# Kernel tuning notes

Measured on AMD Instinct MI355X. Metric: run time of the kernel, lower is better.

The kernel has to match this reference:

```python
import jax, jax.numpy as jnp
import numpy as np

B, D, K, L, C = 1024, 512, 255, 256, 80  # batch, feat, internal nodes, leaves, classes
DEPTH = 8  # complete binary tree: 2^8 = 256 leaves


def _build_res_path():
    # res_path[l, k] = 1 if internal node k is on leaf l's path and leaf goes left,
    # -1 if it goes right, 0 if node k not on the path (matches build_tree_squeeze).
    rp = np.zeros((L, K), dtype=np.int32)
    for leaf in range(L):
        node = 0
        for d in range(DEPTH):
            bit = (leaf >> (DEPTH - 1 - d)) & 1  # 0 -> left, 1 -> right
            rp[leaf, node] = 1 if bit == 0 else -1
            node = 2 * node + 1 + bit
    return jnp.asarray(rp)


def setup_inputs() -> dict:
    key = jax.random.key(0)
    k1, k2, k3, k4 = jax.random.split(key, 4)
    x = jax.random.normal(k1, (B, D), dtype=jnp.float32)
    node_embeddings = jax.random.normal(k2, (K, D), dtype=jnp.float32)
    leaf_W = jax.random.normal(k3, (L * C, D), dtype=jnp.float32) * (1.0 / np.sqrt(D))
    leaf_b = jax.random.normal(k4, (L * C,), dtype=jnp.float32) * 0.01
    res_path = _build_res_path()
    return {"x": x, "node_embeddings": node_embeddings, "leaf_W": leaf_W,
            "leaf_b": leaf_b, "res_path": res_path}


def reference(x, node_embeddings, leaf_W, leaf_b, res_path):
    # L2-normalize node embeddings, cosine-sim routing probabilities
    ne = node_embeddings / jnp.linalg.norm(node_embeddings, axis=-1, keepdims=True)
    node_sim = jax.nn.sigmoid(jnp.einsum('bc,kc->bk', x, ne))  # [B, K]
    # leaf decision logits: Linear(D, L*C) reshaped to [B, L, C]
    leaf_dec = (jnp.einsum('bc,oc->bo', x, leaf_W) + leaf_b).reshape(x.shape[0], L, C)
    left_mask = (res_path == 1)[None]    # [1, L, K]
    right_mask = (res_path == -1)[None]  # [1, L, K]
    ns = node_sim[:, None, :]            # [B, 1, K]
    prob_left = jnp.prod(jnp.where(left_mask, ns, 1.0), axis=-1)        # [B, L]
    prob_right = jnp.prod(jnp.where(right_mask, 1.0 - ns, 1.0), axis=-1)  # [B, L]
    probs = (prob_left * prob_right)[..., None] * leaf_dec  # [B, L, C]
    return probs.sum(axis=1), node_sim
```

## Files before the change

### kernel.cpp

```cpp
#include <hip/hip_runtime.h>
#include <stdint.h>

#define B_  1024
#define D_  512
#define K_  255
#define L_  256
#define C_  80

typedef __attribute__((ext_vector_type(8))) short bf16x8;
typedef __attribute__((ext_vector_type(4))) float f32x4;
typedef __attribute__((ext_vector_type(8))) short short8;

#define GLD(gsrc, ldst) \
  __builtin_amdgcn_global_load_lds((const __attribute__((address_space(1))) void*)(gsrc), \
                                   (__attribute__((address_space(3))) void*)(ldst), 16, 0, 0)

__device__ __forceinline__ short cvt_bf16(float f) {
    unsigned u = __float_as_uint(f);
    u += 0x7FFFu + ((u >> 16) & 1u);
    return (short)(u >> 16);
}

__global__ __launch_bounds__(256) void convert_kernel(const float* __restrict__ w,
                                                      const float* __restrict__ x,
                                                      const float* __restrict__ ne,
                                                      short* __restrict__ wb,
                                                      short* __restrict__ xb,
                                                      short* __restrict__ neb) {
    __shared__ float red[256];
    const int tid = threadIdx.x;
    if (blockIdx.x < 2048) {
        size_t i0 = (size_t)blockIdx.x * 256 + tid;
        const size_t stride = 2048u * 256u;
        for (size_t v = i0; v < 1310720u; v += stride) {
            float4 a = ((const float4*)w)[v * 2];
            float4 b = ((const float4*)w)[v * 2 + 1];
            short8 o;
            o[0] = cvt_bf16(a.x); o[1] = cvt_bf16(a.y); o[2] = cvt_bf16(a.z); o[3] = cvt_bf16(a.w);
            o[4] = cvt_bf16(b.x); o[5] = cvt_bf16(b.y); o[6] = cvt_bf16(b.z); o[7] = cvt_bf16(b.w);
            ((short8*)wb)[v] = o;
        }
        for (size_t v = i0; v < 65536u; v += stride) {
            float4 a = ((const float4*)x)[v * 2];
            float4 b = ((const float4*)x)[v * 2 + 1];
            short8 o;
            o[0] = cvt_bf16(a.x); o[1] = cvt_bf16(a.y); o[2] = cvt_bf16(a.z); o[3] = cvt_bf16(a.w);
            o[4] = cvt_bf16(b.x); o[5] = cvt_bf16(b.y); o[6] = cvt_bf16(b.z); o[7] = cvt_bf16(b.w);
            ((short8*)xb)[v] = o;
        }
    } else {
        const int row = blockIdx.x - 2048;
        if (row == 255) {
            ((unsigned*)(neb + 255 * 512))[tid] = 0u;
            return;
        }
        const float2* nr = (const float2*)(ne + (size_t)row * 512);
        float2 a = nr[tid];
        red[tid] = a.x * a.x + a.y * a.y;
        __syncthreads();
        #pragma unroll
        for (int s = 128; s > 0; s >>= 1) {
            if (tid < s) red[tid] += red[tid + s];
            __syncthreads();
        }
        float inv = rsqrtf(red[0]);
        unsigned lo = (unsigned short)cvt_bf16(a.x * inv);
        unsigned hi = (unsigned short)cvt_bf16(a.y * inv);
        ((unsigned*)(neb + (size_t)row * 512))[tid] = lo | (hi << 16);
    }
}

__global__ __launch_bounds__(256) void simgemm_kernel(const short* __restrict__ xb,
                                                      const short* __restrict__ neb,
                                                      float* __restrict__ out1) {
    __shared__ __align__(16) short Ald[512 * 8];
    __shared__ __align__(16) short Bld[512 * 8];
    const int tid = threadIdx.x;
    const int lane = tid & 63, wave = tid >> 6;
    const int q = lane >> 4, r = lane & 15;
    const int mt = blockIdx.x >> 2;
    const int nt = blockIdx.x & 3;

    f32x4 acc[4];
    #pragma unroll
    for (int nf = 0; nf < 4; ++nf) acc[nf] = (f32x4){0.f, 0.f, 0.f, 0.f};

    const bf16x8* Av = (const bf16x8*)Ald;
    const bf16x8* Bv = (const bf16x8*)Bld;

    for (int kb = 0; kb < 8; ++kb) {
        __syncthreads();
        #pragma unroll
        for (int j = 0; j < 2; ++j) {
            int ph = j * 256 + tid, rr = ph >> 3, g = (ph & 7) ^ (rr & 7);
            GLD(xb + ((size_t)(mt * 64 + rr) * D_ + kb * 64 + g * 8), Ald + ph * 8);
        }
        #pragma unroll
        for (int j = 0; j < 2; ++j) {
            int ph = j * 256 + tid, cc = ph >> 3, g = (ph & 7) ^ (cc & 7);
            GLD(neb + ((size_t)(nt * 64 + cc) * D_ + kb * 64 + g * 8), Bld + ph * 8);
        }
        __syncthreads();
        #pragma unroll
        for (int ks = 0; ks < 2; ++ks) {
            const int g = ks * 4 + q;
            int rl = wave * 16 + r;
            bf16x8 af = Av[rl * 8 + (g ^ (rl & 7))];
            #pragma unroll
            for (int nf = 0; nf < 4; ++nf) {
                int cl = nf * 16 + r;
                bf16x8 bfr = Bv[cl * 8 + (g ^ (cl & 7))];
                acc[nf] = __builtin_amdgcn_mfma_f32_16x16x32_bf16(af, bfr, acc[nf], 0, 0, 0);
            }
        }
    }
    #pragma unroll
    for (int nf = 0; nf < 4; ++nf) {
        int gcol = nt * 64 + nf * 16 + r;
        if (gcol < K_) {
            #pragma unroll
            for (int i = 0; i < 4; ++i) {
                int grow = mt * 64 + wave * 16 + q * 4 + i;
                out1[(size_t)grow * K_ + gcol] = 1.f / (1.f + __expf(-acc[nf][i]));
            }
        }
    }
}

__global__ __launch_bounds__(256) void leafprob_kernel(const float* __restrict__ out1,
                                                       float* __restrict__ p_ws) {
    __shared__ float ss[K_];
    const int b = blockIdx.x, t = threadIdx.x;
    if (t < K_) ss[t] = out1[(size_t)b * K_ + t];
    __syncthreads();
    float prob = 1.f;
    int node = 0;
    #pragma unroll
    for (int d = 0; d < 8; ++d) {
        int bit = (t >> (7 - d)) & 1;
        float s = ss[node];
        prob *= bit ? (1.f - s) : s;
        node = 2 * node + 1 + bit;
    }
    p_ws[(size_t)b * L_ + t] = prob;
}

__global__ __launch_bounds__(256, 2) void gemm_kernel(const short* __restrict__ xb,
                                                      const short* __restrict__ wb,
                                                      const float* __restrict__ p,
                                                      const float* __restrict__ lb,
                                                      float* __restrict__ partial) {
    __shared__ __align__(16) short Ald[1024 * 8];
    __shared__ __align__(16) short Bld[1280 * 8];
    __shared__ float p_ld[128][2];
    __shared__ float b_ld[160];

    const int tid = threadIdx.x;
    const int lane = tid & 63, wave = tid >> 6;
    const int q = lane >> 4, r = lane & 15;
    const int wrow = wave * 32;
    const int lp = blockIdx.x & 127;
    const int mt = blockIdx.x >> 7;

    if (tid < 128) {
        p_ld[tid][0] = p[(size_t)(mt * 128 + tid) * L_ + 2 * lp];
        p_ld[tid][1] = p[(size_t)(mt * 128 + tid) * L_ + 2 * lp + 1];
    }
    if (tid < 160) b_ld[tid] = lb[lp * 160 + tid];

    f32x4 outacc[2][5];
    #pragma unroll
    for (int mf = 0; mf < 2; ++mf)
        #pragma unroll
        for (int nf = 0; nf < 5; ++nf)
            outacc[mf][nf] = (f32x4){0.f, 0.f, 0.f, 0.f};

    const bf16x8* Av = (const bf16x8*)Ald;
    const bf16x8* Bv = (const bf16x8*)Bld;

    for (int kb = 0; kb < 8; ++kb) {
        __syncthreads();
        #pragma unroll
        for (int j = 0; j < 4; ++j) {
            int ph = j * 256 + tid;
            int rr = ph >> 3;
            int g  = (ph & 7) ^ (rr & 7);
            GLD(xb + ((size_t)(mt * 128 + rr) * D_ + kb * 64 + g * 8), Ald + ph * 8);
        }
        #pragma unroll
        for (int j = 0; j < 5; ++j) {
            int ph = j * 256 + tid;
            int cc = ph >> 3;
            int g  = (ph & 7) ^ (cc & 7);
            GLD(wb + ((size_t)(lp * 160 + cc) * D_ + kb * 64 + g * 8), Bld + ph * 8);
        }
        __syncthreads();

        #pragma unroll
        for (int li = 0; li < 2; ++li) {
            f32x4 dec[2][5];
            #pragma unroll
            for (int mf = 0; mf < 2; ++mf)
                #pragma unroll
                for (int nf = 0; nf < 5; ++nf)
                    dec[mf][nf] = (f32x4){0.f, 0.f, 0.f, 0.f};

            #pragma unroll
            for (int ks = 0; ks < 2; ++ks) {
                const int g = ks * 4 + q;
                bf16x8 af[2], bfr[5];
                #pragma unroll
                for (int mf = 0; mf < 2; ++mf) {
                    int rl = wrow + mf * 16 + r;
                    af[mf] = Av[rl * 8 + (g ^ (rl & 7))];
                }
                #pragma unroll
                for (int nf = 0; nf < 5; ++nf) {
                    int cl = li * 80 + nf * 16 + r;
                    bfr[nf] = Bv[cl * 8 + (g ^ (cl & 7))];
                }
                #pragma unroll
                for (int mf = 0; mf < 2; ++mf)
                    #pragma unroll
                    for (int nf = 0; nf < 5; ++nf)
                        dec[mf][nf] = __builtin_amdgcn_mfma_f32_16x16x32_bf16(
                            af[mf], bfr[nf], dec[mf][nf], 0, 0, 0);
            }

            #pragma unroll
            for (int mf = 0; mf < 2; ++mf)
                #pragma unroll
                for (int nf = 0; nf < 5; ++nf)
                    #pragma unroll
                    for (int i = 0; i < 4; ++i) {
                        int row = wrow + mf * 16 + q * 4 + i;
                        outacc[mf][nf][i] += p_ld[row][li] * dec[mf][nf][i];
                    }
        }
    }

    const size_t rbase = (size_t)lp * B_ + mt * 128;
    #pragma unroll
    for (int mf = 0; mf < 2; ++mf)
        #pragma unroll
        for (int nf = 0; nf < 5; ++nf) {
            int col = nf * 16 + r;
            float b0 = b_ld[col], b1 = b_ld[80 + col];
            #pragma unroll
            for (int i = 0; i < 4; ++i) {
                int row = wrow + mf * 16 + q * 4 + i;
                float v = outacc[mf][nf][i] + p_ld[row][0] * b0 + p_ld[row][1] * b1;
                partial[(rbase + row) * C_ + col] = v;
            }
        }
}

__global__ __launch_bounds__(256) void reduce_kernel(const float* __restrict__ partial,
                                                     float* __restrict__ out0) {
    int idx = blockIdx.x * 256 + threadIdx.x;
    const float4* p4 = (const float4*)partial;
    float4 s = {0.f, 0.f, 0.f, 0.f};
    #pragma unroll 8
    for (int j = 0; j < 128; ++j) {
        float4 v = p4[(size_t)j * (B_ * C_ / 4) + idx];
        s.x += v.x; s.y += v.y; s.z += v.z; s.w += v.w;
    }
    ((float4*)out0)[idx] = s;
}

extern "C" void kernel_launch(void* const* d_in, const int* in_sizes, int n_in,
                              void* d_out, int out_size, void* d_ws, size_t ws_size,
                              hipStream_t stream) {
    const float* x  = (const float*)d_in[0];
    const float* ne = (const float*)d_in[1];
    const float* lW = (const float*)d_in[2];
    const float* lb = (const float*)d_in[3];

    float* out0 = (float*)d_out;
    float* out1 = out0 + (size_t)B_ * C_;

    char* ws = (char*)d_ws;
    short* xb      = (short*)ws;
    short* neb     = (short*)(ws + (1u << 20));
    float* p_ws    = (float*)(ws + (1u << 20) + (1u << 18));
    short* wb      = (short*)(ws + (9u << 18));
    float* partial = (float*)(ws + (24u << 20));

    convert_kernel<<<2304, 256, 0, stream>>>(lW, x, ne, wb, xb, neb);
    simgemm_kernel<<<64, 256, 0, stream>>>(xb, neb, out1);
    leafprob_kernel<<<B_, 256, 0, stream>>>(out1, p_ws);
    gemm_kernel<<<1024, 256, 0, stream>>>(xb, wb, p_ws, lb, partial);
    reduce_kernel<<<B_ * C_ / 1024, 256, 0, stream>>>(partial, out0);
}
```

Before: 143.5 us.

## Drop LDS staging in leaf GEMM; load MFMA fragments directly from global memory

Removes the shared-memory tiles and their barriers from the leaf GEMM. Each wave now loads its bf16 A/B fragments directly from global memory and keeps the routing probabilities in registers. The per-chunk MFMA accumulation is replaced by a zero-initialised MFMA per 32-wide k-step, with the probability scaling applied after every step. Occupancy is raised to 3 blocks per SM. The change relies on L1/L2 to serve operand reuse across waves and trades a short accumulation chain for many more scaling FMAs and uncoalesced 16-byte gathers.

```diff
diff --git a/kernel.cpp b/kernel.cpp
--- a/kernel.cpp
+++ b/kernel.cpp
@@ -145,28 +145,31 @@
     p_ws[(size_t)b * L_ + t] = prob;
 }
 
-__global__ __launch_bounds__(256, 2) void gemm_kernel(const short* __restrict__ xb,
+__global__ __launch_bounds__(256, 3) void gemm_kernel(const short* __restrict__ xb,
                                                       const short* __restrict__ wb,
                                                       const float* __restrict__ p,
                                                       const float* __restrict__ lb,
                                                       float* __restrict__ partial) {
-    __shared__ __align__(16) short Ald[1024 * 8];
-    __shared__ __align__(16) short Bld[1280 * 8];
-    __shared__ float p_ld[128][2];
-    __shared__ float b_ld[160];
-
-    const int tid = threadIdx.x;
+    const int tid  = threadIdx.x;
     const int lane = tid & 63, wave = tid >> 6;
     const int q = lane >> 4, r = lane & 15;
     const int wrow = wave * 32;
     const int lp = blockIdx.x & 127;
     const int mt = blockIdx.x >> 7;
 
-    if (tid < 128) {
-        p_ld[tid][0] = p[(size_t)(mt * 128 + tid) * L_ + 2 * lp];
-        p_ld[tid][1] = p[(size_t)(mt * 128 + tid) * L_ + 2 * lp + 1];
-    }
-    if (tid < 160) b_ld[tid] = lb[lp * 160 + tid];
+    float pv[2][2][4];
+    #pragma unroll
+    for (int mf = 0; mf < 2; ++mf)
+        #pragma unroll
+        for (int i = 0; i < 4; ++i) {
+            const float* pr = p + (size_t)(mt * 128 + wrow + mf * 16 + q * 4 + i) * L_ + 2 * lp;
+            pv[mf][0][i] = pr[0];
+            pv[mf][1][i] = pr[1];
+        }
+
+    const short* Ab = xb + (size_t)(mt * 128 + wrow) * D_;
+    const short* Bb = wb + (size_t)lp * 160 * D_;
+    const int voff = r * D_ + q * 8;
 
     f32x4 outacc[2][5];
     #pragma unroll
@@ -175,82 +178,46 @@
         for (int nf = 0; nf < 5; ++nf)
             outacc[mf][nf] = (f32x4){0.f, 0.f, 0.f, 0.f};
 
-    const bf16x8* Av = (const bf16x8*)Ald;
-    const bf16x8* Bv = (const bf16x8*)Bld;
-
-    for (int kb = 0; kb < 8; ++kb) {
-        __syncthreads();
-        #pragma unroll
-        for (int j = 0; j < 4; ++j) {
-            int ph = j * 256 + tid;
-            int rr = ph >> 3;
-            int g  = (ph & 7) ^ (rr & 7);
-            GLD(xb + ((size_t)(mt * 128 + rr) * D_ + kb * 64 + g * 8), Ald + ph * 8);
-        }
-        #pragma unroll
-        for (int j = 0; j < 5; ++j) {
-            int ph = j * 256 + tid;
-            int cc = ph >> 3;
-            int g  = (ph & 7) ^ (cc & 7);
-            GLD(wb + ((size_t)(lp * 160 + cc) * D_ + kb * 64 + g * 8), Bld + ph * 8);
-        }
-        __syncthreads();
-
+    const f32x4 z = {0.f, 0.f, 0.f, 0.f};
+
+    #pragma unroll
+    for (int ks = 0; ks < 16; ++ks) {
+        bf16x8 af[2];
+        #pragma unroll
+        for (int mf = 0; mf < 2; ++mf)
+            af[mf] = *(const bf16x8*)(Ab + mf * 16 * D_ + ks * 32 + voff);
         #pragma unroll
         for (int li = 0; li < 2; ++li) {
-            f32x4 dec[2][5];
+            bf16x8 bfr[5];
+            #pragma unroll
+            for (int nf = 0; nf < 5; ++nf)
+                bfr[nf] = *(const bf16x8*)(Bb + (li * 80 + nf * 16) * D_ + ks * 32 + voff);
             #pragma unroll
             for (int mf = 0; mf < 2; ++mf)
                 #pragma unroll
-                for (int nf = 0; nf < 5; ++nf)
-                    dec[mf][nf] = (f32x4){0.f, 0.f, 0.f, 0.f};
-
-            #pragma unroll
-            for (int ks = 0; ks < 2; ++ks) {
-                const int g = ks * 4 + q;
-                bf16x8 af[2], bfr[5];
-                #pragma unroll
-                for (int mf = 0; mf < 2; ++mf) {
-                    int rl = wrow + mf * 16 + r;
-                    af[mf] = Av[rl * 8 + (g ^ (rl & 7))];
+                for (int nf = 0; nf < 5; ++nf) {
+                    f32x4 dec = __builtin_amdgcn_mfma_f32_16x16x32_bf16(
+                        af[mf], bfr[nf], z, 0, 0, 0);
+                    #pragma unroll
+                    for (int i = 0; i < 4; ++i)
+                        outacc[mf][nf][i] += pv[mf][li][i] * dec[i];
                 }
-                #pragma unroll
-                for (int nf = 0; nf < 5; ++nf) {
-                    int cl = li * 80 + nf * 16 + r;
-                    bfr[nf] = Bv[cl * 8 + (g ^ (cl & 7))];
-                }
-                #pragma unroll
-                for (int mf = 0; mf < 2; ++mf)
-                    #pragma unroll
-                    for (int nf = 0; nf < 5; ++nf)
-                        dec[mf][nf] = __builtin_amdgcn_mfma_f32_16x16x32_bf16(
-                            af[mf], bfr[nf], dec[mf][nf], 0, 0, 0);
-            }
-
-            #pragma unroll
-            for (int mf = 0; mf < 2; ++mf)
-                #pragma unroll
-                for (int nf = 0; nf < 5; ++nf)
-                    #pragma unroll
-                    for (int i = 0; i < 4; ++i) {
-                        int row = wrow + mf * 16 + q * 4 + i;
-                        outacc[mf][nf][i] += p_ld[row][li] * dec[mf][nf][i];
-                    }
-        }
-    }
-
+        }
+    }
+
+    const float* lbb = lb + lp * 160;
     const size_t rbase = (size_t)lp * B_ + mt * 128;
     #pragma unroll
     for (int mf = 0; mf < 2; ++mf)
         #pragma unroll
         for (int nf = 0; nf < 5; ++nf) {
             int col = nf * 16 + r;
-            float b0 = b_ld[col], b1 = b_ld[80 + col];
+            float b0 = lbb[col], b1 = lbb[80 + col];
             #pragma unroll
             for (int i = 0; i < 4; ++i) {
                 int row = wrow + mf * 16 + q * 4 + i;
-                float v = outacc[mf][nf][i] + p_ld[row][0] * b0 + p_ld[row][1] * b1;
-                partial[(rbase + row) * C_ + col] = v;
+                partial[(rbase + row) * C_ + col] =
+                    outacc[mf][nf][i] + pv[mf][0][i] * b0 + pv[mf][1][i] * b1;
             }
         }
 }
```

New measurement: 200.7 us. 39.9% more time.

## Split leaves across waves, accumulate full-K per leaf, combine pair via LDS

Applied to the files above, without the earlier changes.

Each wave now owns one leaf of the pair and 64 rows. It accumulates the full-K product in registers instead of re-zeroing per k-block and scaling by the leaf probability every block. The two leaves are combined at the end through an LDS scratch buffer that aliases the staging tiles. This removes the per-k-block probability multiply-add work, but it raises accumulator registers from 10 to 20 f32x4 and adds an LDS round trip and extra syncs in the epilogue. It also changes B-fragment reuse, with A fragments now loaded for 4 row tiles per wave.

```diff
diff --git a/kernel.cpp b/kernel.cpp
--- a/kernel.cpp
+++ b/kernel.cpp
@@ -150,15 +150,18 @@
                                                       const float* __restrict__ p,
                                                       const float* __restrict__ lb,
                                                       float* __restrict__ partial) {
-    __shared__ __align__(16) short Ald[1024 * 8];
-    __shared__ __align__(16) short Bld[1280 * 8];
+    __shared__ __align__(16) union {
+        struct { short A[1024 * 8]; short Bst[1280 * 8]; } s;
+        float scr[2][64][81];
+    } u;
     __shared__ float p_ld[128][2];
     __shared__ float b_ld[160];
 
     const int tid = threadIdx.x;
     const int lane = tid & 63, wave = tid >> 6;
     const int q = lane >> 4, r = lane & 15;
-    const int wrow = wave * 32;
+    const int li = wave >> 1;
+    const int wr = (wave & 1) * 64;
     const int lp = blockIdx.x & 127;
     const int mt = blockIdx.x >> 7;
 
@@ -168,15 +171,15 @@
     }
     if (tid < 160) b_ld[tid] = lb[lp * 160 + tid];
 
-    f32x4 outacc[2][5];
-    #pragma unroll
-    for (int mf = 0; mf < 2; ++mf)
+    f32x4 dec[4][5];
+    #pragma unroll
+    for (int mf = 0; mf < 4; ++mf)
         #pragma unroll
         for (int nf = 0; nf < 5; ++nf)
-            outacc[mf][nf] = (f32x4){0.f, 0.f, 0.f, 0.f};
-
-    const bf16x8* Av = (const bf16x8*)Ald;
-    const bf16x8* Bv = (const bf16x8*)Bld;
+            dec[mf][nf] = (f32x4){0.f, 0.f, 0.f, 0.f};
+
+    const bf16x8* Av = (const bf16x8*)u.s.A;
+    const bf16x8* Bv = (const bf16x8*)u.s.Bst;
 
     for (int kb = 0; kb < 8; ++kb) {
         __syncthreads();
@@ -185,74 +188,78 @@
             int ph = j * 256 + tid;
             int rr = ph >> 3;
             int g  = (ph & 7) ^ (rr & 7);
-            GLD(xb + ((size_t)(mt * 128 + rr) * D_ + kb * 64 + g * 8), Ald + ph * 8);
+            GLD(xb + ((size_t)(mt * 128 + rr) * D_ + kb * 64 + g * 8), u.s.A + ph * 8);
         }
         #pragma unroll
         for (int j = 0; j < 5; ++j) {
             int ph = j * 256 + tid;
             int cc = ph >> 3;
             int g  = (ph & 7) ^ (cc & 7);
-            GLD(wb + ((size_t)(lp * 160 + cc) * D_ + kb * 64 + g * 8), Bld + ph * 8);
-        }
-        __syncthreads();
-
-        #pragma unroll
-        for (int li = 0; li < 2; ++li) {
-            f32x4 dec[2][5];
-            #pragma unroll
-            for (int mf = 0; mf < 2; ++mf)
+            GLD(wb + ((size_t)(lp * 160 + cc) * D_ + kb * 64 + g * 8), u.s.Bst + ph * 8);
+        }
+        __syncthreads();
+
+        #pragma unroll
+        for (int ks = 0; ks < 2; ++ks) {
+            const int g = ks * 4 + q;
+            bf16x8 af[4];
+            #pragma unroll
+            for (int mf = 0; mf < 4; ++mf) {
+                int rl = wr + mf * 16 + r;
+                af[mf] = Av[rl * 8 + (g ^ (rl & 7))];
+            }
+            #pragma unroll
+            for (int nf = 0; nf < 5; ++nf) {
+                int cl = li * 80 + nf * 16 + r;
+                bf16x8 bfr = Bv[cl * 8 + (g ^ (cl & 7))];
                 #pragma unroll
-                for (int nf = 0; nf < 5; ++nf)
-                    dec[mf][nf] = (f32x4){0.f, 0.f, 0.f, 0.f};
-
-            #pragma unroll
-            for (int ks = 0; ks < 2; ++ks) {
-                const int g = ks * 4 + q;
-                bf16x8 af[2], bfr[5];
+                for (int mf = 0; mf < 4; ++mf)
+                    dec[mf][nf] = __builtin_amdgcn_mfma_f32_16x16x32_bf16(
+                        af[mf], bfr, dec[mf][nf], 0, 0, 0);
+            }
+        }
+    }
+
+    float pv[4][4];
+    #pragma unroll
+    for (int mf = 0; mf < 4; ++mf)
+        #pragma unroll
+        for (int i = 0; i < 4; ++i)
+            pv[mf][i] = p_ld[wr + mf * 16 + q * 4 + i][li];
+
+    __syncthreads();
+
+    if (li == 1) {
+        #pragma unroll
+        for (int mf = 0; mf < 4; ++mf)
+            #pragma unroll
+            for (int nf = 0; nf < 5; ++nf) {
+                int col = nf * 16 + r;
+                float bv = b_ld[80 + col];
                 #pragma unroll
-                for (int mf = 0; mf < 2; ++mf) {
-                    int rl = wrow + mf * 16 + r;
-                    af[mf] = Av[rl * 8 + (g ^ (rl & 7))];
+                for (int i = 0; i < 4; ++i) {
+                    int rowl = mf * 16 + q * 4 + i;
+                    u.scr[wave & 1][rowl][col] = pv[mf][i] * (dec[mf][nf][i] + bv);
                 }
+            }
+    }
+    __syncthreads();
+    if (li == 0) {
+        const size_t rbase = (size_t)lp * B_ + mt * 128;
+        #pragma unroll
+        for (int mf = 0; mf < 4; ++mf)
+            #pragma unroll
+            for (int nf = 0; nf < 5; ++nf) {
+                int col = nf * 16 + r;
+                float bv = b_ld[col];
                 #pragma unroll
-                for (int nf = 0; nf < 5; ++nf) {
-                    int cl = li * 80 + nf * 16 + r;
-                    bfr[nf] = Bv[cl * 8 + (g ^ (cl & 7))];
+                for (int i = 0; i < 4; ++i) {
+                    int rowl = mf * 16 + q * 4 + i;
+                    float v = pv[mf][i] * (dec[mf][nf][i] + bv) + u.scr[wave & 1][rowl][col];
+                    partial[(rbase + wr + rowl) * C_ + col] = v;
                 }
-                #pragma unroll
-                for (int mf = 0; mf < 2; ++mf)
-                    #pragma unroll
-                    for (int nf = 0; nf < 5; ++nf)
-                        dec[mf][nf] = __builtin_amdgcn_mfma_f32_16x16x32_bf16(
-                            af[mf], bfr[nf], dec[mf][nf], 0, 0, 0);
-            }
-
-            #pragma unroll
-            for (int mf = 0; mf < 2; ++mf)
-                #pragma unroll
-                for (int nf = 0; nf < 5; ++nf)
-                    #pragma unroll
-                    for (int i = 0; i < 4; ++i) {
-                        int row = wrow + mf * 16 + q * 4 + i;
-                        outacc[mf][nf][i] += p_ld[row][li] * dec[mf][nf][i];
-                    }
-        }
-    }
-
-    const size_t rbase = (size_t)lp * B_ + mt * 128;
-    #pragma unroll
-    for (int mf = 0; mf < 2; ++mf)
-        #pragma unroll
-        for (int nf = 0; nf < 5; ++nf) {
-            int col = nf * 16 + r;
-            float b0 = b_ld[col], b1 = b_ld[80 + col];
-            #pragma unroll
-            for (int i = 0; i < 4; ++i) {
-                int row = wrow + mf * 16 + q * 4 + i;
-                float v = outacc[mf][nf][i] + p_ld[row][0] * b0 + p_ld[row][1] * b1;
-                partial[(rbase + row) * C_ + col] = v;
-            }
-        }
+            }
+    }
 }
 
 __global__ __launch_bounds__(256) void reduce_kernel(const float* __restrict__ partial,
```

Result: faster. 137.5 us (-4.1%).
